# Kernel tuning notes

Hardware: AMD Instinct MI355X
Metric: run time of the kernel (lower is better)

## Reference

```python
import math
import jax, jax.numpy as jnp
import numpy as np

POS_DIM = 32


def _fourier_features(pos, dim):
    # pos: [B, M] in [0,1] -> [B, M, dim]
    half = dim // 2
    freqs = jnp.exp(jnp.linspace(0.0, math.log(1000.0), half, dtype=pos.dtype))
    ang = pos[..., None] * freqs                      # [B, M, half]
    out = jnp.concatenate([jnp.sin(ang), jnp.cos(ang)], axis=-1)
    if out.shape[-1] < dim:  # pad if dim is odd (not the case for dim=32)
        pad = jnp.zeros(out.shape[:-1] + (dim - out.shape[-1],), dtype=pos.dtype)
        out = jnp.concatenate([out, pad], axis=-1)
    return out


def setup_inputs() -> dict:
    key = jax.random.key(0)
    k1, k2, k3 = jax.random.split(key, 3)
    B, T, D, M = 8, 8192, 512, 512
    frame_emb = jax.random.normal(k1, (B, T, D), dtype=jnp.float32)
    beat_bounds = jax.random.randint(k2, (B, M, 2), 0, T).astype(jnp.int64)
    # nn.Linear(D + POS_DIM, D): store as [in, out] for x @ W + b
    bound = 1.0 / math.sqrt(D + POS_DIM)
    W = jax.random.uniform(k3, (D + POS_DIM, D), dtype=jnp.float32,
                           minval=-bound, maxval=bound)
    b = jnp.zeros((D,), dtype=jnp.float32)
    return {"frame_emb": frame_emb, "beat_bounds": beat_bounds, "W": W, "b": b}


def reference(frame_emb, beat_bounds, W, b):
    B, T, D = frame_emb.shape
    M = beat_bounds.shape[1]
    dt = frame_emb.dtype

    # clamp bounds exactly as the torch loop does
    s = jnp.clip(beat_bounds[..., 0], 0, T - 1)                 # [B, M]
    e = jnp.maximum(s + 1, jnp.minimum(beat_bounds[..., 1], T))  # [B, M]

    # segment mean via exclusive cumsum: sum(frame_emb[b, s:e]) = cs[e] - cs[s]
    cs = jnp.concatenate(
        [jnp.zeros((B, 1, D), dtype=dt), jnp.cumsum(frame_emb, axis=1)], axis=1
    )  # [B, T+1, D]
    seg_sum = (jnp.take_along_axis(cs, e[..., None], axis=1)
               - jnp.take_along_axis(cs, s[..., None], axis=1))   # [B, M, D]
    counts = (e - s).astype(dt)[..., None]
    out = seg_sum / counts

    # fourier position features over beat index
    pos = (jnp.arange(M, dtype=dt) / max(1, M - 1)).clip(0.0, 1.0)  # [M]
    ff = _fourier_features(jnp.broadcast_to(pos[None, :], (B, M)), POS_DIM)
    out = jnp.concatenate([out, ff], axis=-1) @ W + b               # [B, M, D]
    return out
```

## Files before the change

kernel.cpp:

```cpp
#include <hip/hip_runtime.h>
#include <math.h>

#define B 8
#define T 8192
#define D 512
#define M 512
#define POS 32
#define CHUNK 4
#define NCHUNK (T / CHUNK)
#define GRP 32
#define NGRP (NCHUNK / GRP)
#define BM (B * M)
#define KD 512

typedef __attribute__((ext_vector_type(8))) short short8;
typedef __attribute__((ext_vector_type(4))) short short4v;
typedef __attribute__((ext_vector_type(4))) float floatx4;

static __device__ inline unsigned short f2bf(float f) {
    unsigned int u = __float_as_uint(f);
    unsigned int r = (u + 0x7fffu + ((u >> 16) & 1u)) >> 16;
    return (unsigned short)r;
}
static __device__ inline float bf2f(unsigned short h) {
    return __uint_as_float(((unsigned int)h) << 16);
}

__global__ __launch_bounds__(256) void k_fusedA(const float* __restrict__ fe,
                                                const float* __restrict__ W,
                                                const float* __restrict__ bias,
                                                float* __restrict__ cp,
                                                float* __restrict__ gsum,
                                                short* __restrict__ WhT,
                                                short* __restrict__ WlT,
                                                float* __restrict__ ffout) {
    int blk = blockIdx.x;
    int tid = threadIdx.x;
    if (blk < 256) {
        int gg = (blk << 1) | (tid >> 7);
        int b = gg >> 6;
        int g = gg & 63;
        int ht = tid & 127;
        int d4 = ht << 2;
        const float* src = fe + ((size_t)(b * T + g * (GRP * CHUNK)) * D + d4);
        float* cpb = cp + ((size_t)b * NCHUNK + (size_t)g * GRP) * D + d4;
        float4 acc = {0.f, 0.f, 0.f, 0.f};
#pragma unroll 4
        for (int c = 0; c < GRP; ++c) {
#pragma unroll
            for (int r = 0; r < CHUNK; ++r) {
                float4 v = *(const float4*)(src + (size_t)(c * CHUNK + r) * D);
                acc.x += v.x; acc.y += v.y; acc.z += v.z; acc.w += v.w;
            }
            *(float4*)(cpb + (size_t)c * D) = acc;
        }
        *(float4*)(gsum + ((size_t)b * NGRP + g) * D + d4) = acc;
    } else if (blk < 384) {
        __shared__ float ws[32][65];
        int wb = blk - 256;
        int k0 = (wb & 15) * 32;
        int n0 = (wb >> 4) * 64;
        {
            int kk = tid >> 3;
            int nn = (tid & 7) << 3;
            const float* src = W + (size_t)(k0 + kk) * D + n0 + nn;
            float4 v0 = *(const float4*)src;
            float4 v1 = *(const float4*)(src + 4);
            ws[kk][nn + 0] = v0.x; ws[kk][nn + 1] = v0.y; ws[kk][nn + 2] = v0.z; ws[kk][nn + 3] = v0.w;
            ws[kk][nn + 4] = v1.x; ws[kk][nn + 5] = v1.y; ws[kk][nn + 6] = v1.z; ws[kk][nn + 7] = v1.w;
        }
        __syncthreads();
        int n = tid >> 2;
        int kq = (tid & 3) << 3;
        short8 hv, lv;
#pragma unroll
        for (int j = 0; j < 8; ++j) {
            float w = ws[kq + j][n];
            unsigned short hb = f2bf(w);
            hv[j] = (short)hb;
            lv[j] = (short)f2bf(w - bf2f(hb));
        }
        size_t off = (size_t)(n0 + n) * KD + k0 + kq;
        *(short8*)(WhT + off) = hv;
        *(short8*)(WlT + off) = lv;
    } else {
        int m = ((blk - 384) << 1) + (tid >> 7);
        int n4 = (tid & 127) << 2;
        float pos = (float)m * (1.0f / 511.0f);
        float4 acc = *(const float4*)(bias + n4);
#pragma unroll
        for (int j = 0; j < 16; ++j) {
            float freq = expf(0.46051701859880914f * (float)j);
            float ang = pos * freq;
            float s = sinf(ang), c = cosf(ang);
            float4 wsn = *(const float4*)(W + (size_t)(D + j) * D + n4);
            float4 wcn = *(const float4*)(W + (size_t)(D + 16 + j) * D + n4);
            acc.x += s * wsn.x + c * wcn.x;
            acc.y += s * wsn.y + c * wcn.y;
            acc.z += s * wsn.z + c * wcn.z;
            acc.w += s * wsn.w + c * wcn.w;
        }
        *(float4*)(ffout + (size_t)m * D + n4) = acc;
    }
}

__global__ __launch_bounds__(64) void k_scan_coarse(const float* __restrict__ gsum,
                                                    float* __restrict__ gx) {
    int b = blockIdx.x >> 3;
    int d = ((blockIdx.x & 7) << 6) + threadIdx.x;
    const float* gs = gsum + (size_t)b * NGRP * D + d;
    float* gxp = gx + (size_t)b * (NGRP + 1) * D + d;
    float acc = 0.f;
#pragma unroll
    for (int g = 0; g < NGRP; ++g) {
        gxp[(size_t)g * D] = acc;
        acc += gs[(size_t)g * D];
    }
    gxp[(size_t)NGRP * D] = acc;
}

__global__ __launch_bounds__(128) void k_buildx(const float* __restrict__ fe,
                                                const int* __restrict__ bounds,
                                                const float* __restrict__ cp,
                                                const float* __restrict__ gx,
                                                short* __restrict__ Xh,
                                                short* __restrict__ Xl) {
    int bm = blockIdx.x;
    int b = bm / M;
    int b0 = bounds[bm * 2 + 0];
    int b1 = bounds[bm * 2 + 1];
    int s = min(max(b0, 0), T - 1);
    int e = max(min(b1, T), s + 1);
    int cs_ = s >> 2, ce = e >> 2;
    int d4 = threadIdx.x << 2;

    const float* cpb = cp + (size_t)b * NCHUNK * D;
    const float* gxb = gx + (size_t)b * (NGRP + 1) * D;

    float4 acc = *(const float4*)(gxb + (size_t)(ce >> 5) * D + d4);
    if (ce & 31) {
        float4 v = *(const float4*)(cpb + (size_t)(ce - 1) * D + d4);
        acc.x += v.x; acc.y += v.y; acc.z += v.z; acc.w += v.w;
    }
    {
        float4 p = *(const float4*)(gxb + (size_t)(cs_ >> 5) * D + d4);
        acc.x -= p.x; acc.y -= p.y; acc.z -= p.z; acc.w -= p.w;
        if (cs_ & 31) {
            float4 v = *(const float4*)(cpb + (size_t)(cs_ - 1) * D + d4);
            acc.x -= v.x; acc.y -= v.y; acc.z -= v.z; acc.w -= v.w;
        }
    }

    const float* feb = fe + (size_t)b * T * D + d4;
    for (int t = ce * CHUNK; t < e; ++t) {
        float4 v = *(const float4*)(feb + (size_t)t * D);
        acc.x += v.x; acc.y += v.y; acc.z += v.z; acc.w += v.w;
    }
    for (int t = cs_ * CHUNK; t < s; ++t) {
        float4 v = *(const float4*)(feb + (size_t)t * D);
        acc.x -= v.x; acc.y -= v.y; acc.z -= v.z; acc.w -= v.w;
    }
    float inv = 1.0f / (float)(e - s);
    float x0 = acc.x * inv, x1 = acc.y * inv, x2 = acc.z * inv, x3 = acc.w * inv;

    unsigned short h0 = f2bf(x0), h1 = f2bf(x1), h2 = f2bf(x2), h3 = f2bf(x3);
    short4v hv, lv;
    hv[0] = (short)h0; hv[1] = (short)h1; hv[2] = (short)h2; hv[3] = (short)h3;
    lv[0] = (short)f2bf(x0 - bf2f(h0));
    lv[1] = (short)f2bf(x1 - bf2f(h1));
    lv[2] = (short)f2bf(x2 - bf2f(h2));
    lv[3] = (short)f2bf(x3 - bf2f(h3));
    size_t off = (size_t)bm * KD + d4;
    *(short4v*)(Xh + off) = hv;
    *(short4v*)(Xl + off) = lv;
}

#define BK 64
__global__ __launch_bounds__(256) void k_gemm(const short* __restrict__ Xh,
                                              const short* __restrict__ Xl,
                                              const short* __restrict__ WhT,
                                              const short* __restrict__ WlT,
                                              const float* __restrict__ ffout,
                                              float* __restrict__ out) {
    __shared__ short Ah[2][64 * 32], Al[2][64 * 32];
    __shared__ short Bh[2][64 * 32], Bl[2][64 * 32];
    int n0 = (blockIdx.x & 7) << 6;
    int m0 = (blockIdx.x >> 3) << 6;
    int tid = threadIdx.x;
    int w = tid >> 6;
    int l = tid & 63;
    int lm = l & 15;
    int q = l >> 4;
    int wm = (w & 1) << 5;
    int wn = (w >> 1) << 5;

    floatx4 acc[2][2];
#pragma unroll
    for (int i = 0; i < 2; ++i)
#pragma unroll
        for (int j = 0; j < 2; ++j)
            acc[i][j] = (floatx4){0.f, 0.f, 0.f, 0.f};

    int srow = tid >> 2;
    int skq = tid & 3;
    int sslot = skq ^ ((srow >> 1) & 3);
    int ldsoff = (srow << 5) + (sslot << 3);
    const short* gXh = Xh + (size_t)(m0 + srow) * KD + (skq << 3);
    const short* gXl = Xl + (size_t)(m0 + srow) * KD + (skq << 3);
    const short* gBh = WhT + (size_t)(n0 + srow) * KD + (skq << 3);
    const short* gBl = WlT + (size_t)(n0 + srow) * KD + (skq << 3);

    int aoff[2], boff[2];
#pragma unroll
    for (int mt = 0; mt < 2; ++mt) {
        int row = wm + (mt << 4) + lm;
        aoff[mt] = (row << 5) + ((q ^ ((row >> 1) & 3)) << 3);
    }
#pragma unroll
    for (int nt = 0; nt < 2; ++nt) {
        int row = wn + (nt << 4) + lm;
        boff[nt] = (row << 5) + ((q ^ ((row >> 1) & 3)) << 3);
    }

    short8 pxh[2], pxl[2], pbh[2], pbl[2];
#pragma unroll
    for (int h = 0; h < 2; ++h) {
        pxh[h] = *(const short8*)(gXh + (h << 5));
        pxl[h] = *(const short8*)(gXl + (h << 5));
        pbh[h] = *(const short8*)(gBh + (h << 5));
        pbl[h] = *(const short8*)(gBl + (h << 5));
    }

    for (int k0 = 0; k0 < KD; k0 += BK) {
        __syncthreads();
#pragma unroll
        for (int h = 0; h < 2; ++h) {
            *(short8*)(&Ah[h][ldsoff]) = pxh[h];
            *(short8*)(&Al[h][ldsoff]) = pxl[h];
            *(short8*)(&Bh[h][ldsoff]) = pbh[h];
            *(short8*)(&Bl[h][ldsoff]) = pbl[h];
        }
        __syncthreads();

        int kn = k0 + BK;
        if (kn < KD) {
#pragma unroll
            for (int h = 0; h < 2; ++h) {
                pxh[h] = *(const short8*)(gXh + kn + (h << 5));
                pxl[h] = *(const short8*)(gXl + kn + (h << 5));
                pbh[h] = *(const short8*)(gBh + kn + (h << 5));
                pbl[h] = *(const short8*)(gBl + kn + (h << 5));
            }
        }

#pragma unroll
        for (int h = 0; h < 2; ++h) {
            short8 ah[2], al[2], bh[2], bl[2];
#pragma unroll
            for (int mt = 0; mt < 2; ++mt) {
                ah[mt] = *(const short8*)(&Ah[h][aoff[mt]]);
                al[mt] = *(const short8*)(&Al[h][aoff[mt]]);
            }
#pragma unroll
            for (int nt = 0; nt < 2; ++nt) {
                bh[nt] = *(const short8*)(&Bh[h][boff[nt]]);
                bl[nt] = *(const short8*)(&Bl[h][boff[nt]]);
            }
#pragma unroll
            for (int mt = 0; mt < 2; ++mt)
#pragma unroll
                for (int nt = 0; nt < 2; ++nt) {
                    acc[mt][nt] = __builtin_amdgcn_mfma_f32_16x16x32_bf16(
                        ah[mt], bh[nt], acc[mt][nt], 0, 0, 0);
                    acc[mt][nt] = __builtin_amdgcn_mfma_f32_16x16x32_bf16(
                        ah[mt], bl[nt], acc[mt][nt], 0, 0, 0);
                    acc[mt][nt] = __builtin_amdgcn_mfma_f32_16x16x32_bf16(
                        al[mt], bh[nt], acc[mt][nt], 0, 0, 0);
                }
        }
    }

#pragma unroll
    for (int mt = 0; mt < 2; ++mt) {
#pragma unroll
        for (int nt = 0; nt < 2; ++nt) {
            int gcol = n0 + wn + (nt << 4) + lm;
#pragma unroll
            for (int r = 0; r < 4; ++r) {
                int grow = m0 + wm + (mt << 4) + (q << 2) + r;
                float f = ffout[(size_t)(grow & (M - 1)) * D + gcol];
                out[(size_t)grow * D + gcol] = acc[mt][nt][r] + f;
            }
        }
    }
}

extern "C" void kernel_launch(void* const* d_in, const int* in_sizes, int n_in,
                              void* d_out, int out_size, void* d_ws, size_t ws_size,
                              hipStream_t stream) {
    const float* fe = (const float*)d_in[0];
    const int* bounds = (const int*)d_in[1];
    const float* W = (const float*)d_in[2];
    const float* bias = (const float*)d_in[3];
    float* out = (float*)d_out;

    float* cp = (float*)d_ws;
    float* gsum = cp + (size_t)B * NCHUNK * D;
    float* gx = gsum + (size_t)B * NGRP * D;
    float* ffout = gx + (size_t)B * (NGRP + 1) * D;
    short* Xh = (short*)(ffout + (size_t)M * D);
    short* Xl = Xh + (size_t)BM * KD;
    short* WhT = Xl + (size_t)BM * KD;
    short* WlT = WhT + (size_t)KD * D;

    k_fusedA<<<640, 256, 0, stream>>>(fe, W, bias, cp, gsum, WhT, WlT, ffout);
    k_scan_coarse<<<B * 8, 64, 0, stream>>>(gsum, gx);
    k_buildx<<<BM, 128, 0, stream>>>(fe, bounds, cp, gx, Xh, Xl);
    k_gemm<<<64 * 8, 256, 0, stream>>>(Xh, Xl, WhT, WlT, ffout, out);
}
```

Before: 227.8 us.

## Fuse all four kernels into one persistent kernel with grid barriers

Merges the prefix-sum, coarse scan, segment-mean build and split-bf16 GEMM into a single 512-block kernel. The stages are separated by atomic-counter grid barriers, and the counter is reset by a memset before launch. The aim is to remove three kernel launch gaps and the tail effects between stages. In exchange it depends on all 512 blocks being co-resident, and a spin timeout bounds the barrier wait. Work is also remapped: the fourier stage uses 8 columns per thread, and each block builds 8 X rows instead of one row per block.

Measured after the change: 392.7 us. +72.4%, slower.

```diff
diff --git a/kernel.cpp b/kernel.cpp
--- a/kernel.cpp
+++ b/kernel.cpp
@@ -5,13 +5,13 @@
 #define T 8192
 #define D 512
 #define M 512
-#define POS 32
 #define CHUNK 4
 #define NCHUNK (T / CHUNK)
 #define GRP 32
 #define NGRP (NCHUNK / GRP)
 #define BM (B * M)
 #define KD 512
+#define NBLK 512
 
 typedef __attribute__((ext_vector_type(8))) short short8;
 typedef __attribute__((ext_vector_type(4))) short short4v;
@@ -26,22 +26,39 @@
     return __uint_as_float(((unsigned int)h) << 16);
 }
 
-__global__ __launch_bounds__(256) void k_fusedA(const float* __restrict__ fe,
-                                                const float* __restrict__ W,
-                                                const float* __restrict__ bias,
-                                                float* __restrict__ cp,
-                                                float* __restrict__ gsum,
-                                                short* __restrict__ WhT,
-                                                short* __restrict__ WlT,
-                                                float* __restrict__ ffout) {
+static __device__ inline void gridbar(unsigned* bar) {
+    __syncthreads();
+    if (threadIdx.x == 0) {
+        __threadfence();
+        atomicAdd(bar, 1u);
+        unsigned spins = 0;
+        while (__hip_atomic_load(bar, __ATOMIC_RELAXED,
+                                 __HIP_MEMORY_SCOPE_AGENT) < NBLK) {
+            __builtin_amdgcn_s_sleep(8);
+            if (++spins > 2000000u) break;
+        }
+        __threadfence();
+    }
+    __syncthreads();
+}
+
+__global__ __launch_bounds__(256, 2) void k_all(
+        const float* __restrict__ fe, const int* __restrict__ bounds,
+        const float* __restrict__ W, const float* __restrict__ bias,
+        float* __restrict__ cp, float* __restrict__ gsum,
+        float* __restrict__ gx, float* __restrict__ ffout,
+        short* __restrict__ Xh, short* __restrict__ Xl,
+        short* __restrict__ WhT, short* __restrict__ WlT,
+        unsigned* __restrict__ bar, float* __restrict__ out) {
+    __shared__ __align__(16) char smem[32768];
     int blk = blockIdx.x;
     int tid = threadIdx.x;
+
     if (blk < 256) {
         int gg = (blk << 1) | (tid >> 7);
         int b = gg >> 6;
         int g = gg & 63;
-        int ht = tid & 127;
-        int d4 = ht << 2;
+        int d4 = (tid & 127) << 2;
         const float* src = fe + ((size_t)(b * T + g * (GRP * CHUNK)) * D + d4);
         float* cpb = cp + ((size_t)b * NCHUNK + (size_t)g * GRP) * D + d4;
         float4 acc = {0.f, 0.f, 0.f, 0.f};
@@ -56,7 +73,7 @@
         }
         *(float4*)(gsum + ((size_t)b * NGRP + g) * D + d4) = acc;
     } else if (blk < 384) {
-        __shared__ float ws[32][65];
+        float (*ws)[65] = (float (*)[65])smem;
         int wb = blk - 256;
         int k0 = (wb & 15) * 32;
         int n0 = (wb >> 4) * 64;
@@ -84,212 +101,221 @@
         *(short8*)(WhT + off) = hv;
         *(short8*)(WlT + off) = lv;
     } else {
-        int m = ((blk - 384) << 1) + (tid >> 7);
-        int n4 = (tid & 127) << 2;
+        int m = ((blk - 384) << 2) + (tid >> 6);
+        int n8 = (tid & 63) << 3;
         float pos = (float)m * (1.0f / 511.0f);
-        float4 acc = *(const float4*)(bias + n4);
+        float4 a0 = *(const float4*)(bias + n8);
+        float4 a1 = *(const float4*)(bias + n8 + 4);
 #pragma unroll
         for (int j = 0; j < 16; ++j) {
             float freq = expf(0.46051701859880914f * (float)j);
             float ang = pos * freq;
             float s = sinf(ang), c = cosf(ang);
-            float4 wsn = *(const float4*)(W + (size_t)(D + j) * D + n4);
-            float4 wcn = *(const float4*)(W + (size_t)(D + 16 + j) * D + n4);
-            acc.x += s * wsn.x + c * wcn.x;
-            acc.y += s * wsn.y + c * wcn.y;
-            acc.z += s * wsn.z + c * wcn.z;
-            acc.w += s * wsn.w + c * wcn.w;
-        }
-        *(float4*)(ffout + (size_t)m * D + n4) = acc;
-    }
-}
-
-__global__ __launch_bounds__(64) void k_scan_coarse(const float* __restrict__ gsum,
-                                                    float* __restrict__ gx) {
-    int b = blockIdx.x >> 3;
-    int d = ((blockIdx.x & 7) << 6) + threadIdx.x;
-    const float* gs = gsum + (size_t)b * NGRP * D + d;
-    float* gxp = gx + (size_t)b * (NGRP + 1) * D + d;
-    float acc = 0.f;
-#pragma unroll
-    for (int g = 0; g < NGRP; ++g) {
-        gxp[(size_t)g * D] = acc;
-        acc += gs[(size_t)g * D];
-    }
-    gxp[(size_t)NGRP * D] = acc;
-}
-
-__global__ __launch_bounds__(128) void k_buildx(const float* __restrict__ fe,
-                                                const int* __restrict__ bounds,
-                                                const float* __restrict__ cp,
-                                                const float* __restrict__ gx,
-                                                short* __restrict__ Xh,
-                                                short* __restrict__ Xl) {
-    int bm = blockIdx.x;
-    int b = bm / M;
-    int b0 = bounds[bm * 2 + 0];
-    int b1 = bounds[bm * 2 + 1];
-    int s = min(max(b0, 0), T - 1);
-    int e = max(min(b1, T), s + 1);
-    int cs_ = s >> 2, ce = e >> 2;
-    int d4 = threadIdx.x << 2;
-
-    const float* cpb = cp + (size_t)b * NCHUNK * D;
-    const float* gxb = gx + (size_t)b * (NGRP + 1) * D;
-
-    float4 acc = *(const float4*)(gxb + (size_t)(ce >> 5) * D + d4);
-    if (ce & 31) {
-        float4 v = *(const float4*)(cpb + (size_t)(ce - 1) * D + d4);
-        acc.x += v.x; acc.y += v.y; acc.z += v.z; acc.w += v.w;
-    }
+            const float* wr = W + (size_t)(D + j) * D + n8;
+            const float* wc = W + (size_t)(D + 16 + j) * D + n8;
+            float4 s0 = *(const float4*)wr;
+            float4 s1 = *(const float4*)(wr + 4);
+            float4 c0 = *(const float4*)wc;
+            float4 c1 = *(const float4*)(wc + 4);
+            a0.x += s * s0.x + c * c0.x;
+            a0.y += s * s0.y + c * c0.y;
+            a0.z += s * s0.z + c * c0.z;
+            a0.w += s * s0.w + c * c0.w;
+            a1.x += s * s1.x + c * c1.x;
+            a1.y += s * s1.y + c * c1.y;
+            a1.z += s * s1.z + c * c1.z;
+            a1.w += s * s1.w + c * c1.w;
+        }
+        *(float4*)(ffout + (size_t)m * D + n8) = a0;
+        *(float4*)(ffout + (size_t)m * D + n8 + 4) = a1;
+    }
+
+    gridbar(bar + 0);
+
+    if (blk < 16) {
+        int b = blk >> 1;
+        int d = ((blk & 1) << 8) + tid;
+        const float* gs = gsum + (size_t)b * NGRP * D + d;
+        float* gxp = gx + (size_t)b * (NGRP + 1) * D + d;
+        float acc = 0.f;
+#pragma unroll
+        for (int g = 0; g < NGRP; ++g) {
+            gxp[(size_t)g * D] = acc;
+            acc += gs[(size_t)g * D];
+        }
+        gxp[(size_t)NGRP * D] = acc;
+    }
+
+    gridbar(bar + 1);
+
     {
-        float4 p = *(const float4*)(gxb + (size_t)(cs_ >> 5) * D + d4);
-        acc.x -= p.x; acc.y -= p.y; acc.z -= p.z; acc.w -= p.w;
-        if (cs_ & 31) {
-            float4 v = *(const float4*)(cpb + (size_t)(cs_ - 1) * D + d4);
-            acc.x -= v.x; acc.y -= v.y; acc.z -= v.z; acc.w -= v.w;
-        }
-    }
-
-    const float* feb = fe + (size_t)b * T * D + d4;
-    for (int t = ce * CHUNK; t < e; ++t) {
-        float4 v = *(const float4*)(feb + (size_t)t * D);
-        acc.x += v.x; acc.y += v.y; acc.z += v.z; acc.w += v.w;
-    }
-    for (int t = cs_ * CHUNK; t < s; ++t) {
-        float4 v = *(const float4*)(feb + (size_t)t * D);
-        acc.x -= v.x; acc.y -= v.y; acc.z -= v.z; acc.w -= v.w;
-    }
-    float inv = 1.0f / (float)(e - s);
-    float x0 = acc.x * inv, x1 = acc.y * inv, x2 = acc.z * inv, x3 = acc.w * inv;
-
-    unsigned short h0 = f2bf(x0), h1 = f2bf(x1), h2 = f2bf(x2), h3 = f2bf(x3);
-    short4v hv, lv;
-    hv[0] = (short)h0; hv[1] = (short)h1; hv[2] = (short)h2; hv[3] = (short)h3;
-    lv[0] = (short)f2bf(x0 - bf2f(h0));
-    lv[1] = (short)f2bf(x1 - bf2f(h1));
-    lv[2] = (short)f2bf(x2 - bf2f(h2));
-    lv[3] = (short)f2bf(x3 - bf2f(h3));
-    size_t off = (size_t)bm * KD + d4;
-    *(short4v*)(Xh + off) = hv;
-    *(short4v*)(Xl + off) = lv;
-}
-
-#define BK 64
-__global__ __launch_bounds__(256) void k_gemm(const short* __restrict__ Xh,
-                                              const short* __restrict__ Xl,
-                                              const short* __restrict__ WhT,
-                                              const short* __restrict__ WlT,
-                                              const float* __restrict__ ffout,
-                                              float* __restrict__ out) {
-    __shared__ short Ah[2][64 * 32], Al[2][64 * 32];
-    __shared__ short Bh[2][64 * 32], Bl[2][64 * 32];
-    int n0 = (blockIdx.x & 7) << 6;
-    int m0 = (blockIdx.x >> 3) << 6;
-    int tid = threadIdx.x;
-    int w = tid >> 6;
-    int l = tid & 63;
-    int lm = l & 15;
-    int q = l >> 4;
-    int wm = (w & 1) << 5;
-    int wn = (w >> 1) << 5;
-
-    floatx4 acc[2][2];
-#pragma unroll
-    for (int i = 0; i < 2; ++i)
-#pragma unroll
-        for (int j = 0; j < 2; ++j)
-            acc[i][j] = (floatx4){0.f, 0.f, 0.f, 0.f};
-
-    int srow = tid >> 2;
-    int skq = tid & 3;
-    int sslot = skq ^ ((srow >> 1) & 3);
-    int ldsoff = (srow << 5) + (sslot << 3);
-    const short* gXh = Xh + (size_t)(m0 + srow) * KD + (skq << 3);
-    const short* gXl = Xl + (size_t)(m0 + srow) * KD + (skq << 3);
-    const short* gBh = WhT + (size_t)(n0 + srow) * KD + (skq << 3);
-    const short* gBl = WlT + (size_t)(n0 + srow) * KD + (skq << 3);
-
-    int aoff[2], boff[2];
+        int ht = tid & 127;
+        int d4 = ht << 2;
+#pragma unroll
+        for (int r = 0; r < 4; ++r) {
+            int bm = (blk << 3) + (r << 1) + (tid >> 7);
+            int b = bm >> 9;
+            int b0 = bounds[bm * 2 + 0];
+            int b1 = bounds[bm * 2 + 1];
+            int s = min(max(b0, 0), T - 1);
+            int e = max(min(b1, T), s + 1);
+            int cs_ = s >> 2, ce = e >> 2;
+
+            const float* cpb = cp + (size_t)b * NCHUNK * D;
+            const float* gxb = gx + (size_t)b * (NGRP + 1) * D;
+
+            float4 acc = *(const float4*)(gxb + (size_t)(ce >> 5) * D + d4);
+            if (ce & 31) {
+                float4 v = *(const float4*)(cpb + (size_t)(ce - 1) * D + d4);
+                acc.x += v.x; acc.y += v.y; acc.z += v.z; acc.w += v.w;
+            }
+            {
+                float4 p = *(const float4*)(gxb + (size_t)(cs_ >> 5) * D + d4);
+                acc.x -= p.x; acc.y -= p.y; acc.z -= p.z; acc.w -= p.w;
+                if (cs_ & 31) {
+                    float4 v = *(const float4*)(cpb + (size_t)(cs_ - 1) * D + d4);
+                    acc.x -= v.x; acc.y -= v.y; acc.z -= v.z; acc.w -= v.w;
+                }
+            }
+            const float* feb = fe + (size_t)b * T * D + d4;
+            for (int t = ce * CHUNK; t < e; ++t) {
+                float4 v = *(const float4*)(feb + (size_t)t * D);
+                acc.x += v.x; acc.y += v.y; acc.z += v.z; acc.w += v.w;
+            }
+            for (int t = cs_ * CHUNK; t < s; ++t) {
+                float4 v = *(const float4*)(feb + (size_t)t * D);
+                acc.x -= v.x; acc.y -= v.y; acc.z -= v.z; acc.w -= v.w;
+            }
+            float inv = 1.0f / (float)(e - s);
+            float x0 = acc.x * inv, x1 = acc.y * inv, x2 = acc.z * inv, x3 = acc.w * inv;
+
+            unsigned short h0 = f2bf(x0), h1 = f2bf(x1), h2 = f2bf(x2), h3 = f2bf(x3);
+            short4v hv, lv;
+            hv[0] = (short)h0; hv[1] = (short)h1; hv[2] = (short)h2; hv[3] = (short)h3;
+            lv[0] = (short)f2bf(x0 - bf2f(h0));
+            lv[1] = (short)f2bf(x1 - bf2f(h1));
+            lv[2] = (short)f2bf(x2 - bf2f(h2));
+            lv[3] = (short)f2bf(x3 - bf2f(h3));
+            size_t off = (size_t)bm * KD + d4;
+            *(short4v*)(Xh + off) = hv;
+            *(short4v*)(Xl + off) = lv;
+        }
+    }
+
+    gridbar(bar + 2);
+
+    {
+        short* Ah0 = (short*)smem;
+        short* Al0 = Ah0 + 4096;
+        short* Bh0 = Al0 + 4096;
+        short* Bl0 = Bh0 + 4096;
+
+        int n0 = (blk & 7) << 6;
+        int m0 = (blk >> 3) << 6;
+        int w = tid >> 6;
+        int l = tid & 63;
+        int lm = l & 15;
+        int q = l >> 4;
+        int wm = (w & 1) << 5;
+        int wn = (w >> 1) << 5;
+
+        floatx4 acc[2][2];
+#pragma unroll
+        for (int i = 0; i < 2; ++i)
+#pragma unroll
+            for (int j = 0; j < 2; ++j)
+                acc[i][j] = (floatx4){0.f, 0.f, 0.f, 0.f};
+
+        int srow = tid >> 2;
+        int skq = tid & 3;
+        int sslot = skq ^ ((srow >> 1) & 3);
+        int ldsoff = (srow << 5) + (sslot << 3);
+        const short* gXh = Xh + (size_t)(m0 + srow) * KD + (skq << 3);
+        const short* gXl = Xl + (size_t)(m0 + srow) * KD + (skq << 3);
+        const short* gBh = WhT + (size_t)(n0 + srow) * KD + (skq << 3);
+        const short* gBl = WlT + (size_t)(n0 + srow) * KD + (skq << 3);
+
+        int aoff[2], boff[2];
+#pragma unroll
+        for (int mt = 0; mt < 2; ++mt) {
+            int row = wm + (mt << 4) + lm;
+            aoff[mt] = (row << 5) + ((q ^ ((row >> 1) & 3)) << 3);
+        }
+#pragma unroll
+        for (int nt = 0; nt < 2; ++nt) {
+            int row = wn + (nt << 4) + lm;
+            boff[nt] = (row << 5) + ((q ^ ((row >> 1) & 3)) << 3);
+        }
+
+        short8 pxh[2], pxl[2], pbh[2], pbl[2];
+#pragma unroll
+        for (int h = 0; h < 2; ++h) {
+            pxh[h] = *(const short8*)(gXh + (h << 5));
+            pxl[h] = *(const short8*)(gXl + (h << 5));
+            pbh[h] = *(const short8*)(gBh + (h << 5));
+            pbl[h] = *(const short8*)(gBl + (h << 5));
+        }
+
+        for (int k0 = 0; k0 < KD; k0 += 64) {
+            __syncthreads();
+#pragma unroll
+            for (int h = 0; h < 2; ++h) {
+                *(short8*)(&Ah0[(h << 11) + ldsoff]) = pxh[h];
+                *(short8*)(&Al0[(h << 11) + ldsoff]) = pxl[h];
+                *(short8*)(&Bh0[(h << 11) + ldsoff]) = pbh[h];
+                *(short8*)(&Bl0[(h << 11) + ldsoff]) = pbl[h];
+            }
+            __syncthreads();
+
+            int kn = k0 + 64;
+            if (kn < KD) {
+#pragma unroll
+                for (int h = 0; h < 2; ++h) {
+                    pxh[h] = *(const short8*)(gXh + kn + (h << 5));
+                    pxl[h] = *(const short8*)(gXl + kn + (h << 5));
+                    pbh[h] = *(const short8*)(gBh + kn + (h << 5));
+                    pbl[h] = *(const short8*)(gBl + kn + (h << 5));
+                }
+            }
+
+#pragma unroll
+            for (int h = 0; h < 2; ++h) {
+                short8 ah[2], al[2], bh[2], bl[2];
+#pragma unroll
+                for (int mt = 0; mt < 2; ++mt) {
+                    ah[mt] = *(const short8*)(&Ah0[(h << 11) + aoff[mt]]);
+                    al[mt] = *(const short8*)(&Al0[(h << 11) + aoff[mt]]);
+                }
+#pragma unroll
+                for (int nt = 0; nt < 2; ++nt) {
+                    bh[nt] = *(const short8*)(&Bh0[(h << 11) + boff[nt]]);
+                    bl[nt] = *(const short8*)(&Bl0[(h << 11) + boff[nt]]);
+                }
+#pragma unroll
+                for (int mt = 0; mt < 2; ++mt)
+#pragma unroll
+                    for (int nt = 0; nt < 2; ++nt) {
+                        acc[mt][nt] = __builtin_amdgcn_mfma_f32_16x16x32_bf16(
+                            ah[mt], bh[nt], acc[mt][nt], 0, 0, 0);
+                        acc[mt][nt] = __builtin_amdgcn_mfma_f32_16x16x32_bf16(
+                            ah[mt], bl[nt], acc[mt][nt], 0, 0, 0);
+                        acc[mt][nt] = __builtin_amdgcn_mfma_f32_16x16x32_bf16(
+                            al[mt], bh[nt], acc[mt][nt], 0, 0, 0);
+                    }
+            }
+        }
+
 #pragma unroll
     for (int mt = 0; mt < 2; ++mt) {
-        int row = wm + (mt << 4) + lm;
-        aoff[mt] = (row << 5) + ((q ^ ((row >> 1) & 3)) << 3);
-    }
-#pragma unroll
-    for (int nt = 0; nt < 2; ++nt) {
-        int row = wn + (nt << 4) + lm;
-        boff[nt] = (row << 5) + ((q ^ ((row >> 1) & 3)) << 3);
-    }
-
-    short8 pxh[2], pxl[2], pbh[2], pbl[2];
-#pragma unroll
-    for (int h = 0; h < 2; ++h) {
-        pxh[h] = *(const short8*)(gXh + (h << 5));
-        pxl[h] = *(const short8*)(gXl + (h << 5));
-        pbh[h] = *(const short8*)(gBh + (h << 5));
-        pbl[h] = *(const short8*)(gBl + (h << 5));
-    }
-
-    for (int k0 = 0; k0 < KD; k0 += BK) {
-        __syncthreads();
-#pragma unroll
-        for (int h = 0; h < 2; ++h) {
-            *(short8*)(&Ah[h][ldsoff]) = pxh[h];
-            *(short8*)(&Al[h][ldsoff]) = pxl[h];
-            *(short8*)(&Bh[h][ldsoff]) = pbh[h];
-            *(short8*)(&Bl[h][ldsoff]) = pbl[h];
-        }
-        __syncthreads();
-
-        int kn = k0 + BK;
-        if (kn < KD) {
-#pragma unroll
-            for (int h = 0; h < 2; ++h) {
-                pxh[h] = *(const short8*)(gXh + kn + (h << 5));
-                pxl[h] = *(const short8*)(gXl + kn + (h << 5));
-                pbh[h] = *(const short8*)(gBh + kn + (h << 5));
-                pbl[h] = *(const short8*)(gBl + kn + (h << 5));
-            }
-        }
-
-#pragma unroll
-        for (int h = 0; h < 2; ++h) {
-            short8 ah[2], al[2], bh[2], bl[2];
-#pragma unroll
-            for (int mt = 0; mt < 2; ++mt) {
-                ah[mt] = *(const short8*)(&Ah[h][aoff[mt]]);
-                al[mt] = *(const short8*)(&Al[h][aoff[mt]]);
-            }
 #pragma unroll
             for (int nt = 0; nt < 2; ++nt) {
-                bh[nt] = *(const short8*)(&Bh[h][boff[nt]]);
-                bl[nt] = *(const short8*)(&Bl[h][boff[nt]]);
-            }
-#pragma unroll
-            for (int mt = 0; mt < 2; ++mt)
-#pragma unroll
-                for (int nt = 0; nt < 2; ++nt) {
-                    acc[mt][nt] = __builtin_amdgcn_mfma_f32_16x16x32_bf16(
-                        ah[mt], bh[nt], acc[mt][nt], 0, 0, 0);
-                    acc[mt][nt] = __builtin_amdgcn_mfma_f32_16x16x32_bf16(
-                        ah[mt], bl[nt], acc[mt][nt], 0, 0, 0);
-                    acc[mt][nt] = __builtin_amdgcn_mfma_f32_16x16x32_bf16(
-                        al[mt], bh[nt], acc[mt][nt], 0, 0, 0);
-                }
-        }
-    }
-
-#pragma unroll
-    for (int mt = 0; mt < 2; ++mt) {
-#pragma unroll
-        for (int nt = 0; nt < 2; ++nt) {
-            int gcol = n0 + wn + (nt << 4) + lm;
-#pragma unroll
-            for (int r = 0; r < 4; ++r) {
-                int grow = m0 + wm + (mt << 4) + (q << 2) + r;
-                float f = ffout[(size_t)(grow & (M - 1)) * D + gcol];
-                out[(size_t)grow * D + gcol] = acc[mt][nt][r] + f;
+                int gcol = n0 + wn + (nt << 4) + lm;
+#pragma unroll
+                for (int r = 0; r < 4; ++r) {
+                    int grow = m0 + wm + (mt << 4) + (q << 2) + r;
+                    float f = ffout[(size_t)(grow & (M - 1)) * D + gcol];
+                    out[(size_t)grow * D + gcol] = acc[mt][nt][r] + f;
+                }
             }
         }
     }
@@ -312,9 +338,9 @@
     short* Xl = Xh + (size_t)BM * KD;
     short* WhT = Xl + (size_t)BM * KD;
     short* WlT = WhT + (size_t)KD * D;
-
-    k_fusedA<<<640, 256, 0, stream>>>(fe, W, bias, cp, gsum, WhT, WlT, ffout);
-    k_scan_coarse<<<B * 8, 64, 0, stream>>>(gsum, gx);
-    k_buildx<<<BM, 128, 0, stream>>>(fe, bounds, cp, gx, Xh, Xl);
-    k_gemm<<<64 * 8, 256, 0, stream>>>(Xh, Xl, WhT, WlT, ffout, out);
-}
+    unsigned* bar = (unsigned*)(WlT + (size_t)KD * D);
+
+    hipMemsetAsync(bar, 0, 64, stream);
+    k_all<<<NBLK, 256, 0, stream>>>(fe, bounds, W, bias, cp, gsum, gx, ffout,
+                                    Xh, Xl, WhT, WlT, bar, out);
+}
```

## Use single bf16 GEMM instead of split hi/lo and inline coarse scan

Applied to the files above, without the earlier changes.

Drops the hi/lo bf16 split of X and W, so the GEMM issues one MFMA per tile instead of three and reads half the operand data. The coarse scan kernel is removed; buildx instead sums group totals directly per segment. This removes a launch and the lo-part conversions and stores, at the cost of reduced accuracy (plain bf16 operands) and redundant group-sum reads per row.

After: 231.0 us. No clear change (+1.4%).

```diff
diff --git a/kernel.cpp b/kernel.cpp
--- a/kernel.cpp
+++ b/kernel.cpp
@@ -5,7 +5,6 @@
 #define T 8192
 #define D 512
 #define M 512
-#define POS 32
 #define CHUNK 4
 #define NCHUNK (T / CHUNK)
 #define GRP 32
@@ -22,9 +21,6 @@
     unsigned int r = (u + 0x7fffu + ((u >> 16) & 1u)) >> 16;
     return (unsigned short)r;
 }
-static __device__ inline float bf2f(unsigned short h) {
-    return __uint_as_float(((unsigned int)h) << 16);
-}
 
 __global__ __launch_bounds__(256) void k_fusedA(const float* __restrict__ fe,
                                                 const float* __restrict__ W,
@@ -32,7 +28,6 @@
                                                 float* __restrict__ cp,
                                                 float* __restrict__ gsum,
                                                 short* __restrict__ WhT,
-                                                short* __restrict__ WlT,
                                                 float* __restrict__ ffout) {
     int blk = blockIdx.x;
     int tid = threadIdx.x;
@@ -72,17 +67,12 @@
         __syncthreads();
         int n = tid >> 2;
         int kq = (tid & 3) << 3;
-        short8 hv, lv;
+        short8 hv;
 #pragma unroll
         for (int j = 0; j < 8; ++j) {
-            float w = ws[kq + j][n];
-            unsigned short hb = f2bf(w);
-            hv[j] = (short)hb;
-            lv[j] = (short)f2bf(w - bf2f(hb));
-        }
-        size_t off = (size_t)(n0 + n) * KD + k0 + kq;
-        *(short8*)(WhT + off) = hv;
-        *(short8*)(WlT + off) = lv;
+            hv[j] = (short)f2bf(ws[kq + j][n]);
+        }
+        *(short8*)(WhT + (size_t)(n0 + n) * KD + k0 + kq) = hv;
     } else {
         int m = ((blk - 384) << 1) + (tid >> 7);
         int n4 = (tid & 127) << 2;
@@ -104,51 +94,43 @@
     }
 }
 
-__global__ __launch_bounds__(64) void k_scan_coarse(const float* __restrict__ gsum,
-                                                    float* __restrict__ gx) {
-    int b = blockIdx.x >> 3;
-    int d = ((blockIdx.x & 7) << 6) + threadIdx.x;
-    const float* gs = gsum + (size_t)b * NGRP * D + d;
-    float* gxp = gx + (size_t)b * (NGRP + 1) * D + d;
-    float acc = 0.f;
-#pragma unroll
-    for (int g = 0; g < NGRP; ++g) {
-        gxp[(size_t)g * D] = acc;
-        acc += gs[(size_t)g * D];
-    }
-    gxp[(size_t)NGRP * D] = acc;
-}
-
 __global__ __launch_bounds__(128) void k_buildx(const float* __restrict__ fe,
                                                 const int* __restrict__ bounds,
                                                 const float* __restrict__ cp,
-                                                const float* __restrict__ gx,
-                                                short* __restrict__ Xh,
-                                                short* __restrict__ Xl) {
+                                                const float* __restrict__ gsum,
+                                                short* __restrict__ X) {
     int bm = blockIdx.x;
-    int b = bm / M;
+    int b = bm >> 9;
     int b0 = bounds[bm * 2 + 0];
     int b1 = bounds[bm * 2 + 1];
     int s = min(max(b0, 0), T - 1);
     int e = max(min(b1, T), s + 1);
     int cs_ = s >> 2, ce = e >> 2;
+    int gcs = cs_ >> 5, gce = ce >> 5;
     int d4 = threadIdx.x << 2;
 
     const float* cpb = cp + (size_t)b * NCHUNK * D;
-    const float* gxb = gx + (size_t)b * (NGRP + 1) * D;
-
-    float4 acc = *(const float4*)(gxb + (size_t)(ce >> 5) * D + d4);
+    const float* gsb = gsum + (size_t)b * NGRP * D + d4;
+
+    float4 acc = {0.f, 0.f, 0.f, 0.f};
+    int g = 0;
+    for (; g < gcs; ++g) {
+        float4 v = *(const float4*)(gsb + (size_t)g * D);
+        acc.x += v.x; acc.y += v.y; acc.z += v.z; acc.w += v.w;
+    }
+    float4 pcs = acc;
+    for (; g < gce; ++g) {
+        float4 v = *(const float4*)(gsb + (size_t)g * D);
+        acc.x += v.x; acc.y += v.y; acc.z += v.z; acc.w += v.w;
+    }
     if (ce & 31) {
         float4 v = *(const float4*)(cpb + (size_t)(ce - 1) * D + d4);
         acc.x += v.x; acc.y += v.y; acc.z += v.z; acc.w += v.w;
     }
-    {
-        float4 p = *(const float4*)(gxb + (size_t)(cs_ >> 5) * D + d4);
-        acc.x -= p.x; acc.y -= p.y; acc.z -= p.z; acc.w -= p.w;
-        if (cs_ & 31) {
-            float4 v = *(const float4*)(cpb + (size_t)(cs_ - 1) * D + d4);
-            acc.x -= v.x; acc.y -= v.y; acc.z -= v.z; acc.w -= v.w;
-        }
+    acc.x -= pcs.x; acc.y -= pcs.y; acc.z -= pcs.z; acc.w -= pcs.w;
+    if (cs_ & 31) {
+        float4 v = *(const float4*)(cpb + (size_t)(cs_ - 1) * D + d4);
+        acc.x -= v.x; acc.y -= v.y; acc.z -= v.z; acc.w -= v.w;
     }
 
     const float* feb = fe + (size_t)b * T * D + d4;
@@ -161,29 +143,21 @@
         acc.x -= v.x; acc.y -= v.y; acc.z -= v.z; acc.w -= v.w;
     }
     float inv = 1.0f / (float)(e - s);
-    float x0 = acc.x * inv, x1 = acc.y * inv, x2 = acc.z * inv, x3 = acc.w * inv;
-
-    unsigned short h0 = f2bf(x0), h1 = f2bf(x1), h2 = f2bf(x2), h3 = f2bf(x3);
-    short4v hv, lv;
-    hv[0] = (short)h0; hv[1] = (short)h1; hv[2] = (short)h2; hv[3] = (short)h3;
-    lv[0] = (short)f2bf(x0 - bf2f(h0));
-    lv[1] = (short)f2bf(x1 - bf2f(h1));
-    lv[2] = (short)f2bf(x2 - bf2f(h2));
-    lv[3] = (short)f2bf(x3 - bf2f(h3));
-    size_t off = (size_t)bm * KD + d4;
-    *(short4v*)(Xh + off) = hv;
-    *(short4v*)(Xl + off) = lv;
+    short4v hv;
+    hv[0] = (short)f2bf(acc.x * inv);
+    hv[1] = (short)f2bf(acc.y * inv);
+    hv[2] = (short)f2bf(acc.z * inv);
+    hv[3] = (short)f2bf(acc.w * inv);
+    *(short4v*)(X + (size_t)bm * KD + d4) = hv;
 }
 
 #define BK 64
-__global__ __launch_bounds__(256) void k_gemm(const short* __restrict__ Xh,
-                                              const short* __restrict__ Xl,
+__global__ __launch_bounds__(256) void k_gemm(const short* __restrict__ X,
                                               const short* __restrict__ WhT,
-                                              const short* __restrict__ WlT,
                                               const float* __restrict__ ffout,
                                               float* __restrict__ out) {
-    __shared__ short Ah[2][64 * 32], Al[2][64 * 32];
-    __shared__ short Bh[2][64 * 32], Bl[2][64 * 32];
+    __shared__ short Ah[2][64 * 32];
+    __shared__ short Bh[2][64 * 32];
     int n0 = (blockIdx.x & 7) << 6;
     int m0 = (blockIdx.x >> 3) << 6;
     int tid = threadIdx.x;
@@ -205,10 +179,8 @@
     int skq = tid & 3;
     int sslot = skq ^ ((srow >> 1) & 3);
     int ldsoff = (srow << 5) + (sslot << 3);
-    const short* gXh = Xh + (size_t)(m0 + srow) * KD + (skq << 3);
-    const short* gXl = Xl + (size_t)(m0 + srow) * KD + (skq << 3);
-    const short* gBh = WhT + (size_t)(n0 + srow) * KD + (skq << 3);
-    const short* gBl = WlT + (size_t)(n0 + srow) * KD + (skq << 3);
+    const short* gX = X + (size_t)(m0 + srow) * KD + (skq << 3);
+    const short* gB = WhT + (size_t)(n0 + srow) * KD + (skq << 3);
 
     int aoff[2], boff[2];
 #pragma unroll
@@ -222,13 +194,11 @@
         boff[nt] = (row << 5) + ((q ^ ((row >> 1) & 3)) << 3);
     }
 
-    short8 pxh[2], pxl[2], pbh[2], pbl[2];
+    short8 pxh[2], pbh[2];
 #pragma unroll
     for (int h = 0; h < 2; ++h) {
-        pxh[h] = *(const short8*)(gXh + (h << 5));
-        pxl[h] = *(const short8*)(gXl + (h << 5));
-        pbh[h] = *(const short8*)(gBh + (h << 5));
-        pbl[h] = *(const short8*)(gBl + (h << 5));
+        pxh[h] = *(const short8*)(gX + (h << 5));
+        pbh[h] = *(const short8*)(gB + (h << 5));
     }
 
     for (int k0 = 0; k0 < KD; k0 += BK) {
@@ -236,9 +206,7 @@
 #pragma unroll
         for (int h = 0; h < 2; ++h) {
             *(short8*)(&Ah[h][ldsoff]) = pxh[h];
-            *(short8*)(&Al[h][ldsoff]) = pxl[h];
             *(short8*)(&Bh[h][ldsoff]) = pbh[h];
-            *(short8*)(&Bl[h][ldsoff]) = pbl[h];
         }
         __syncthreads();
 
@@ -246,37 +214,26 @@
         if (kn < KD) {
 #pragma unroll
             for (int h = 0; h < 2; ++h) {
-                pxh[h] = *(const short8*)(gXh + kn + (h << 5));
-                pxl[h] = *(const short8*)(gXl + kn + (h << 5));
-                pbh[h] = *(const short8*)(gBh + kn + (h << 5));
-                pbl[h] = *(const short8*)(gBl + kn + (h << 5));
+                pxh[h] = *(const short8*)(gX + kn + (h << 5));
+                pbh[h] = *(const short8*)(gB + kn + (h << 5));
             }
         }
 
 #pragma unroll
         for (int h = 0; h < 2; ++h) {
-            short8 ah[2], al[2], bh[2], bl[2];
-#pragma unroll
-            for (int mt = 0; mt < 2; ++mt) {
+            short8 ah[2], bh[2];
+#pragma unroll
+            for (int mt = 0; mt < 2; ++mt)
                 ah[mt] = *(const short8*)(&Ah[h][aoff[mt]]);
-                al[mt] = *(const short8*)(&Al[h][aoff[mt]]);
-            }
-#pragma unroll
-            for (int nt = 0; nt < 2; ++nt) {
+#pragma unroll
+            for (int nt = 0; nt < 2; ++nt)
                 bh[nt] = *(const short8*)(&Bh[h][boff[nt]]);
-                bl[nt] = *(const short8*)(&Bl[h][boff[nt]]);
-            }
 #pragma unroll
             for (int mt = 0; mt < 2; ++mt)
 #pragma unroll
-                for (int nt = 0; nt < 2; ++nt) {
+                for (int nt = 0; nt < 2; ++nt)
                     acc[mt][nt] = __builtin_amdgcn_mfma_f32_16x16x32_bf16(
                         ah[mt], bh[nt], acc[mt][nt], 0, 0, 0);
-                    acc[mt][nt] = __builtin_amdgcn_mfma_f32_16x16x32_bf16(
-                        ah[mt], bl[nt], acc[mt][nt], 0, 0, 0);
-                    acc[mt][nt] = __builtin_amdgcn_mfma_f32_16x16x32_bf16(
-                        al[mt], bh[nt], acc[mt][nt], 0, 0, 0);
-                }
         }
     }
 
@@ -306,15 +263,11 @@
 
     float* cp = (float*)d_ws;
     float* gsum = cp + (size_t)B * NCHUNK * D;
-    float* gx = gsum + (size_t)B * NGRP * D;
-    float* ffout = gx + (size_t)B * (NGRP + 1) * D;
-    short* Xh = (short*)(ffout + (size_t)M * D);
-    short* Xl = Xh + (size_t)BM * KD;
-    short* WhT = Xl + (size_t)BM * KD;
-    short* WlT = WhT + (size_t)KD * D;
-
-    k_fusedA<<<640, 256, 0, stream>>>(fe, W, bias, cp, gsum, WhT, WlT, ffout);
-    k_scan_coarse<<<B * 8, 64, 0, stream>>>(gsum, gx);
-    k_buildx<<<BM, 128, 0, stream>>>(fe, bounds, cp, gx, Xh, Xl);
-    k_gemm<<<64 * 8, 256, 0, stream>>>(Xh, Xl, WhT, WlT, ffout, out);
-}
+    float* ffout = gsum + (size_t)B * NGRP * D;
+    short* X = (short*)(ffout + (size_t)M * D);
+    short* WhT = X + (size_t)BM * KD;
+
+    k_fusedA<<<640, 256, 0, stream>>>(fe, W, bias, cp, gsum, WhT, ffout);
+    k_buildx<<<BM, 128, 0, stream>>>(fe, bounds, cp, gsum, X);
+    k_gemm<<<64 * 8, 256, 0, stream>>>(X, WhT, ffout, out);
+}
```
